# Kernel optimization log

Hardware: AMD Instinct MI355X
Metric: run time of the kernel (lower is better)

Reference implementation:

```python
import jax, jax.numpy as jnp
import numpy as np

B, M, H, NLAYERS = 32768, 32, 64, 4
DIM_IN = (4 + 1) * M  # 160


def prelu(x, a):
    return jnp.where(x >= 0, x, a * x)


def setup_inputs() -> dict:
    key = jax.random.key(0)
    ks = jax.random.split(key, 10)

    x = jax.random.normal(ks[0], (B, M, 4), dtype=jnp.float32)
    pad_mask = jax.random.randint(ks[1], (B, M), 0, 2).astype(bool)

    def lin(k, fan_out, fan_in):
        bound = 1.0 / np.sqrt(fan_in)
        kw, kb = jax.random.split(k)
        W = jax.random.uniform(kw, (fan_out, fan_in), jnp.float32, -bound, bound)
        b = jax.random.uniform(kb, (fan_out,), jnp.float32, -bound, bound)
        return W, b

    W_in, b_in = lin(ks[2], H, DIM_IN)
    a_in = jnp.full((1,), 0.25, jnp.float32)  # PReLU slope

    enc_W, enc_b = [], []
    for i in range(NLAYERS):
        W, b = lin(ks[3 + i], H, H)
        enc_W.append(W)
        enc_b.append(b)
    W_enc = jnp.stack(enc_W)              # [4, 64, 64]
    b_enc = jnp.stack(enc_b)              # [4, 64]
    a_enc = jnp.full((NLAYERS, 1), 0.25, jnp.float32)

    W_out, b_out = lin(ks[8], M, H)       # [32, 64]

    return {"x": x, "pad_mask": pad_mask, "W_in": W_in, "b_in": b_in,
            "a_in": a_in, "W_enc": W_enc, "b_enc": b_enc, "a_enc": a_enc,
            "W_out": W_out, "b_out": b_out}


def reference(x, pad_mask, W_in, b_in, a_in, W_enc, b_enc, a_enc, W_out, b_out):
    # ---- FullyConnectedNetwork: learn per-satellite weights w [B, M] ----
    valid = (~pad_mask).astype(x.dtype)[..., None]          # [B, M, 1]
    feats = jnp.concatenate([x, valid], axis=-1)            # [B, M, 5]
    feats = feats.reshape(feats.shape[0], -1)               # [B, 5*M] (M == max_sats, pad is no-op)

    h = prelu(feats @ W_in.T + b_in, a_in)                  # [B, 64]
    for i in range(NLAYERS):
        h = prelu(h @ W_enc[i].T + b_enc[i], a_enc[i])
    w = h @ W_out.T + b_out                                  # [B, M]

    # ---- Weighted least squares: diag(w) applied as row-scale (same math as diag_embed + bmm) ----
    ones = jnp.ones(x.shape[:2] + (1,), dtype=x.dtype)
    A = jnp.concatenate([-x[:, :, 1:4], ones], axis=-1)      # [B, M, 4]
    r = x[:, :, 0:1]                                         # [B, M, 1]

    WA = w[:, :, None] * A                                   # [B, M, 4]
    Wr = w[:, :, None] * r                                   # [B, M, 1]

    WA_pinv = jnp.linalg.pinv(WA)                            # [B, 4, M]
    out = jnp.matmul(WA_pinv, Wr)[..., 0]                    # [B, 4]
    return out
```

## Files before the change

kernel.cpp:

```cpp
#include <hip/hip_runtime.h>
#include <cstddef>
#include <cstdint>

typedef float f32x4 __attribute__((ext_vector_type(4)));
typedef __bf16 bf16x8 __attribute__((ext_vector_type(8)));

#define MFMA_B16(a, b, c) __builtin_amdgcn_mfma_f32_16x16x32_bf16(a, b, c, 0, 0, 0)

#define OFF_L0   0u
#define OFF_WV   32768u
#define OFF_ENC  40960u
#define OFF_OUT  106496u
#define WS_NEED  114688u

#define XB_OFF   0
#define AH_OFF   32768
#define AL_OFF   40960
#define WG_OFF   49152

__device__ __forceinline__ int xadr(int e, int b) { return (e << 9) | (b ^ ((e & 7) << 4)); }
__device__ __forceinline__ int aadr(int e, int b) { return (e << 7) | (b ^ ((e & 7) << 4)); }

__global__ __launch_bounds__(256)
void prep_frags(const float* __restrict__ W_in, const float* __restrict__ W_enc,
                const float* __restrict__ W_out, unsigned* __restrict__ P) {
  const int idx = blockIdx.x * 256 + threadIdx.x;
  if (idx >= 28672) return;
  const int t = idx & 3;
  const int lane = (idx >> 2) & 63;
  const int g = lane >> 4, c = lane & 15;
  const int j0 = t << 1;
  int pl;
  float w0, w1;
  if (idx < 8192) {
    const int rest = idx >> 8;
    pl = rest & 1;
    const int nt = (rest >> 1) & 3;
    const int kt = rest >> 3;
    const int n = 4 * c + nt;
    const int k = kt * 32 + g * 8 + j0;
    const int m = k >> 2, q = k & 3;
    w0 = W_in[n * 160 + 5 * m + q];
    w1 = W_in[n * 160 + 5 * m + q + 1];
  } else if (idx < 10240) {
    const int rest = (idx - 8192) >> 8;
    pl = rest & 1;
    const int nt = rest >> 1;
    const int n = 4 * c + nt;
    const int m = g * 8 + j0;
    w0 = W_in[n * 160 + 5 * m + 4];
    w1 = W_in[n * 160 + 5 * (m + 1) + 4];
  } else if (idx < 26624) {
    const int rel = idx - 10240;
    const int l = rel >> 12;
    const int rest = (rel & 4095) >> 8;
    pl = rest & 1;
    const int nt = (rest >> 1) & 3;
    const int kt = rest >> 3;
    const int n = 4 * c + nt;
    const int k = kt * 32 + g * 8 + j0;
    w0 = W_enc[(l * 64 + n) * 64 + k];
    w1 = W_enc[(l * 64 + n) * 64 + k + 1];
  } else {
    const int rel = idx - 26624;
    const int rest = rel >> 8;
    pl = rest & 1;
    const int nt = (rest >> 1) & 1;
    const int kt = rest >> 2;
    const int mcol = 16 * nt + c;
    const int k = kt * 32 + g * 8 + j0;
    w0 = W_out[mcol * 64 + k];
    w1 = W_out[mcol * 64 + k + 1];
  }
  unsigned short u0, u1;
  if (pl == 0) {
    u0 = __builtin_bit_cast(unsigned short, (__bf16)w0);
    u1 = __builtin_bit_cast(unsigned short, (__bf16)w1);
  } else {
    const __bf16 h0 = (__bf16)w0, h1 = (__bf16)w1;
    u0 = __builtin_bit_cast(unsigned short, (__bf16)(w0 - (float)h0));
    u1 = __builtin_bit_cast(unsigned short, (__bf16)(w1 - (float)h1));
  }
  P[idx] = (unsigned)u0 | ((unsigned)u1 << 16);
}

__global__ __launch_bounds__(256, 2)
void wls_mfma(const float* __restrict__ x, const int* __restrict__ pad,
              const float* __restrict__ b_in, const float* __restrict__ a_in,
              const float* __restrict__ b_enc, const float* __restrict__ a_enc,
              const float* __restrict__ b_out, const char* __restrict__ wf,
              float* __restrict__ out) {
  __shared__ __align__(16) unsigned char smem[65536];
  const int tid = threadIdx.x;
  const int wave = tid >> 6, lane = tid & 63;
  const int g = lane >> 4, c = lane & 15;
  const int eb = blockIdx.x << 6;
  const int ew = eb + (wave << 4);

  {
    float4 xv[8];
    const char* src = (const char*)x + (size_t)ew * 512 + lane * 16;
    #pragma unroll
    for (int i = 0; i < 8; ++i) xv[i] = *(const float4*)(src + i * 1024);
    #pragma unroll
    for (int i = 0; i < 8; ++i) {
      const int off = i * 1024 + lane * 16;
      const int e = (wave << 4) + (off >> 9);
      *(float4*)(smem + XB_OFF + xadr(e, off & 511)) = xv[i];
    }
  }
  {
    #pragma unroll
    for (int t = 0; t < 2; ++t) {
      const int el = lane >> 2;
      const int mq = (lane & 3) + (t << 2);
      const int4 pv = *(const int4*)(pad + (size_t)(ew + el) * 32 + (mq << 2));
      const unsigned ONE = 0x3F80u;
      const unsigned u0 = (pv.x ? 0u : ONE) | ((pv.y ? 0u : ONE) << 16);
      const unsigned u1 = (pv.z ? 0u : ONE) | ((pv.w ? 0u : ONE) << 16);
      const int e = (wave << 4) + el;
      *(uint2*)(smem + AL_OFF + aadr(e, mq << 3)) = make_uint2(u0, u1);
    }
  }

  auto copy_wgt = [&](unsigned goff, int nbytes) {
    const int share = nbytes >> 2;
    const char* s = wf + goff + wave * share + lane * 16;
    unsigned char* d = smem + WG_OFF + wave * share + lane * 16;
    if (nbytes == 16384) {
      float4 t0 = *(const float4*)(s);
      float4 t1 = *(const float4*)(s + 1024);
      float4 t2 = *(const float4*)(s + 2048);
      float4 t3 = *(const float4*)(s + 3072);
      *(float4*)(d) = t0;           *(float4*)(d + 1024) = t1;
      *(float4*)(d + 2048) = t2;    *(float4*)(d + 3072) = t3;
    } else {
      float4 t0 = *(const float4*)(s);
      float4 t1 = *(const float4*)(s + 1024);
      *(float4*)(d) = t0;           *(float4*)(d + 1024) = t1;
    }
  };
  auto bfrag = [&](int slot) -> bf16x8 {
    return *(const bf16x8*)(smem + WG_OFF + slot * 1024 + lane * 16);
  };
  auto xfrag = [&](int kt, bf16x8& ah, bf16x8& al) {
    const int e = (wave << 4) + c;
    const int b0 = kt * 128 + g * 32;
    const float4 v0 = *(const float4*)(smem + XB_OFF + xadr(e, b0));
    const float4 v1 = *(const float4*)(smem + XB_OFF + xadr(e, b0 + 16));
    const float vv[8] = {v0.x, v0.y, v0.z, v0.w, v1.x, v1.y, v1.z, v1.w};
    #pragma unroll
    for (int j = 0; j < 8; ++j) {
      const __bf16 h = (__bf16)vv[j];
      ah[j] = h;
      al[j] = (__bf16)(vv[j] - (float)h);
    }
  };
  auto act_store = [&](f32x4* a4, float alpha) {
    #pragma unroll
    for (int r = 0; r < 4; ++r) {
      const int e = (wave << 4) + (g << 2) + r;
      unsigned hu[2], lu[2];
      #pragma unroll
      for (int q = 0; q < 2; ++q) {
        unsigned short hb[2], lb[2];
        #pragma unroll
        for (int s2 = 0; s2 < 2; ++s2) {
          float h = a4[2 * q + s2][r];
          h = (h >= 0.0f) ? h : alpha * h;
          const __bf16 hh = (__bf16)h;
          const __bf16 ll = (__bf16)(h - (float)hh);
          hb[s2] = __builtin_bit_cast(unsigned short, hh);
          lb[s2] = __builtin_bit_cast(unsigned short, ll);
        }
        hu[q] = (unsigned)hb[0] | ((unsigned)hb[1] << 16);
        lu[q] = (unsigned)lb[0] | ((unsigned)lb[1] << 16);
      }
      *(uint2*)(smem + AH_OFF + aadr(e, c * 8)) = make_uint2(hu[0], hu[1]);
      *(uint2*)(smem + AL_OFF + aadr(e, c * 8)) = make_uint2(lu[0], lu[1]);
    }
  };

  f32x4 acc[4];
  #pragma unroll
  for (int nt = 0; nt < 4; ++nt) {
    const float bv = b_in[4 * c + nt];
    f32x4 a = {bv, bv, bv, bv};
    acc[nt] = a;
  }
  copy_wgt(OFF_L0, 16384);
  __syncthreads();
  #pragma unroll
  for (int half = 0; half < 2; ++half) {
    if (half) {
      __syncthreads();
      copy_wgt(OFF_L0 + 16384, 16384);
      __syncthreads();
    }
    #pragma unroll
    for (int ktl = 0; ktl < 2; ++ktl) {
      bf16x8 ah, al;
      xfrag(half * 2 + ktl, ah, al);
      #pragma unroll
      for (int nt = 0; nt < 4; ++nt) {
        const bf16x8 bh = bfrag((ktl * 4 + nt) * 2);
        const bf16x8 bl = bfrag((ktl * 4 + nt) * 2 + 1);
        acc[nt] = MFMA_B16(ah, bh, acc[nt]);
        acc[nt] = MFMA_B16(ah, bl, acc[nt]);
        acc[nt] = MFMA_B16(al, bh, acc[nt]);
      }
    }
  }
  __syncthreads();
  copy_wgt(OFF_WV, 8192);
  __syncthreads();
  {
    const int e = (wave << 4) + c;
    const bf16x8 va = *(const bf16x8*)(smem + AL_OFF + aadr(e, g * 16));
    #pragma unroll
    for (int nt = 0; nt < 4; ++nt) {
      const bf16x8 bh = bfrag(nt * 2);
      const bf16x8 bl = bfrag(nt * 2 + 1);
      acc[nt] = MFMA_B16(va, bh, acc[nt]);
      acc[nt] = MFMA_B16(va, bl, acc[nt]);
    }
  }
  act_store(acc, a_in[0]);

  #pragma unroll
  for (int l = 0; l < 4; ++l) {
    __syncthreads();
    copy_wgt(OFF_ENC + l * 16384, 16384);
    __syncthreads();
    bf16x8 ah0, ah1, al0, al1;
    {
      const int e = (wave << 4) + c;
      ah0 = *(const bf16x8*)(smem + AH_OFF + aadr(e, g * 16));
      ah1 = *(const bf16x8*)(smem + AH_OFF + aadr(e, 64 + g * 16));
      al0 = *(const bf16x8*)(smem + AL_OFF + aadr(e, g * 16));
      al1 = *(const bf16x8*)(smem + AL_OFF + aadr(e, 64 + g * 16));
    }
    f32x4 a2[4];
    #pragma unroll
    for (int nt = 0; nt < 4; ++nt) {
      const float bv = b_enc[l * 64 + 4 * c + nt];
      f32x4 a = {bv, bv, bv, bv};
      a2[nt] = a;
    }
    #pragma unroll
    for (int kt = 0; kt < 2; ++kt) {
      const bf16x8 Ah = kt ? ah1 : ah0;
      const bf16x8 Al = kt ? al1 : al0;
      #pragma unroll
      for (int nt = 0; nt < 4; ++nt) {
        const bf16x8 bh = bfrag((kt * 4 + nt) * 2);
        const bf16x8 bl = bfrag((kt * 4 + nt) * 2 + 1);
        a2[nt] = MFMA_B16(Ah, bh, a2[nt]);
        a2[nt] = MFMA_B16(Ah, bl, a2[nt]);
        a2[nt] = MFMA_B16(Al, bh, a2[nt]);
      }
    }
    act_store(a2, a_enc[l]);
  }

  __syncthreads();
  copy_wgt(OFF_OUT, 8192);
  __syncthreads();
  bf16x8 oah[2], oal[2], obh[4], obl[4];
  {
    const int e = (wave << 4) + c;
    #pragma unroll
    for (int kt = 0; kt < 2; ++kt) {
      oah[kt] = *(const bf16x8*)(smem + AH_OFF + aadr(e, kt * 64 + g * 16));
      oal[kt] = *(const bf16x8*)(smem + AL_OFF + aadr(e, kt * 64 + g * 16));
      #pragma unroll
      for (int nt = 0; nt < 2; ++nt) {
        obh[kt * 2 + nt] = bfrag((kt * 2 + nt) * 2);
        obl[kt * 2 + nt] = bfrag((kt * 2 + nt) * 2 + 1);
      }
    }
  }
  __syncthreads();
  f32x4 aw[2];
  #pragma unroll
  for (int nt = 0; nt < 2; ++nt) {
    const float bv = b_out[16 * nt + c];
    f32x4 a = {bv, bv, bv, bv};
    aw[nt] = a;
  }
  #pragma unroll
  for (int kt = 0; kt < 2; ++kt) {
    #pragma unroll
    for (int nt = 0; nt < 2; ++nt) {
      aw[nt] = MFMA_B16(oah[kt], obh[kt * 2 + nt], aw[nt]);
      aw[nt] = MFMA_B16(oah[kt], obl[kt * 2 + nt], aw[nt]);
      aw[nt] = MFMA_B16(oal[kt], obh[kt * 2 + nt], aw[nt]);
    }
  }
  {
    float* ws = (float*)(smem + WG_OFF);
    #pragma unroll
    for (int nt = 0; nt < 2; ++nt)
      #pragma unroll
      for (int r = 0; r < 4; ++r)
        ws[((wave << 4) + (g << 2) + r) * 33 + 16 * nt + c] = aw[nt][r];
  }

  {
    const int el = lane >> 2;
    const int p = lane & 3;
    const int e = (wave << 4) + el;
    const float* ws = (const float*)(smem + WG_OFF);
    float s[14];
    #pragma unroll
    for (int v = 0; v < 14; ++v) s[v] = 0.0f;
    #pragma unroll
    for (int t = 0; t < 8; ++t) {
      const int mm = (p << 3) + t;
      const float w = ws[e * 33 + mm];
      const float4 xv = *(const float4*)(smem + XB_OFF + xadr(e, mm << 4));
      const float r = xv.x;
      const float a1 = -xv.y, a2 = -xv.z, a3 = -xv.w;
      const float ww = w * w;
      const float w1 = ww * a1, w2 = ww * a2, w3 = ww * a3;
      s[0] += w1 * a1;  s[1] += w1 * a2;  s[2] += w1 * a3;  s[3] += w1;
      s[4] += w2 * a2;  s[5] += w2 * a3;  s[6] += w2;
      s[7] += w3 * a3;  s[8] += w3;
      s[9] += ww;
      s[10] += w1 * r;  s[11] += w2 * r;  s[12] += w3 * r;  s[13] += ww * r;
    }
    #pragma unroll
    for (int v = 0; v < 14; ++v) {
      s[v] += __shfl_xor(s[v], 1);
      s[v] += __shfl_xor(s[v], 2);
    }
    float Mt[4][5] = {
      {s[0], s[1], s[2], s[3], s[10]},
      {s[1], s[4], s[5], s[6], s[11]},
      {s[2], s[5], s[7], s[8], s[12]},
      {s[3], s[6], s[8], s[9], s[13]},
    };
    #pragma unroll
    for (int k = 0; k < 3; ++k) {
      const float inv = 1.0f / Mt[k][k];
      #pragma unroll
      for (int r2 = k + 1; r2 < 4; ++r2) {
        const float fk = Mt[r2][k] * inv;
        #pragma unroll
        for (int cc = k + 1; cc < 5; ++cc) Mt[r2][cc] -= fk * Mt[k][cc];
      }
    }
    const float th3 = Mt[3][4] / Mt[3][3];
    const float th2 = (Mt[2][4] - Mt[2][3] * th3) / Mt[2][2];
    const float th1 = (Mt[1][4] - Mt[1][3] * th3 - Mt[1][2] * th2) / Mt[1][1];
    const float th0 = (Mt[0][4] - Mt[0][3] * th3 - Mt[0][2] * th2 - Mt[0][1] * th1) / Mt[0][0];
    if (p == 0) {
      *(float4*)(out + (size_t)(eb + (wave << 4) + el) * 4) = make_float4(th0, th1, th2, th3);
    }
  }
}

extern "C" void kernel_launch(void* const* d_in, const int* in_sizes, int n_in,
                              void* d_out, int out_size, void* d_ws, size_t ws_size,
                              hipStream_t stream) {
  const float* x     = (const float*)d_in[0];
  const int*   pad   = (const int*)d_in[1];
  const float* W_in  = (const float*)d_in[2];
  const float* b_in  = (const float*)d_in[3];
  const float* a_in  = (const float*)d_in[4];
  const float* W_enc = (const float*)d_in[5];
  const float* b_enc = (const float*)d_in[6];
  const float* a_enc = (const float*)d_in[7];
  const float* W_out = (const float*)d_in[8];
  const float* b_out = (const float*)d_in[9];
  float* out = (float*)d_out;

  prep_frags<<<112, 256, 0, stream>>>(W_in, W_enc, W_out, (unsigned*)d_ws);
  wls_mfma<<<512, 256, 0, stream>>>(x, pad, b_in, a_in, b_enc, a_enc, b_out,
                                    (const char*)d_ws, out);
}
```

Measured before the change: 94.77 us.

## Use single-wave blocks reading weight fragments directly from global memory

Shrinks the block from four waves to one wave handling 16 elements and launches four times as many blocks. Weight fragments are no longer staged through LDS with block barriers; each MFMA operand is loaded straight from global memory, relying on L1/L2 caching. This cuts LDS use to about 14 KB and removes all __syncthreads, aiming for higher occupancy and less barrier stalling. The cost is more global and cache traffic for the weight fragments, since every wave fetches them independently.

```diff
diff --git a/kernel.cpp b/kernel.cpp
--- a/kernel.cpp
+++ b/kernel.cpp
@@ -11,12 +11,12 @@
 #define OFF_WV   32768u
 #define OFF_ENC  40960u
 #define OFF_OUT  106496u
-#define WS_NEED  114688u
 
 #define XB_OFF   0
-#define AH_OFF   32768
-#define AL_OFF   40960
-#define WG_OFF   49152
+#define AH_OFF   8192
+#define AL_OFF   10240
+#define WS_OFF   12288
+#define SMEM_SZ  14400
 
 __device__ __forceinline__ int xadr(int e, int b) { return (e << 9) | (b ^ ((e & 7) << 4)); }
 __device__ __forceinline__ int aadr(int e, int b) { return (e << 7) | (b ^ ((e & 7) << 4)); }
@@ -84,18 +84,16 @@
   P[idx] = (unsigned)u0 | ((unsigned)u1 << 16);
 }
 
-__global__ __launch_bounds__(256, 2)
+__global__ __launch_bounds__(64)
 void wls_mfma(const float* __restrict__ x, const int* __restrict__ pad,
               const float* __restrict__ b_in, const float* __restrict__ a_in,
               const float* __restrict__ b_enc, const float* __restrict__ a_enc,
               const float* __restrict__ b_out, const char* __restrict__ wf,
               float* __restrict__ out) {
-  __shared__ __align__(16) unsigned char smem[65536];
-  const int tid = threadIdx.x;
-  const int wave = tid >> 6, lane = tid & 63;
+  __shared__ __align__(16) unsigned char smem[SMEM_SZ];
+  const int lane = threadIdx.x;
   const int g = lane >> 4, c = lane & 15;
-  const int eb = blockIdx.x << 6;
-  const int ew = eb + (wave << 4);
+  const int ew = blockIdx.x << 4;
 
   {
     float4 xv[8];
@@ -105,8 +103,7 @@
     #pragma unroll
     for (int i = 0; i < 8; ++i) {
       const int off = i * 1024 + lane * 16;
-      const int e = (wave << 4) + (off >> 9);
-      *(float4*)(smem + XB_OFF + xadr(e, off & 511)) = xv[i];
+      *(float4*)(smem + XB_OFF + xadr(off >> 9, off & 511)) = xv[i];
     }
   }
   {
@@ -118,36 +115,17 @@
       const unsigned ONE = 0x3F80u;
       const unsigned u0 = (pv.x ? 0u : ONE) | ((pv.y ? 0u : ONE) << 16);
       const unsigned u1 = (pv.z ? 0u : ONE) | ((pv.w ? 0u : ONE) << 16);
-      const int e = (wave << 4) + el;
-      *(uint2*)(smem + AL_OFF + aadr(e, mq << 3)) = make_uint2(u0, u1);
-    }
-  }
-
-  auto copy_wgt = [&](unsigned goff, int nbytes) {
-    const int share = nbytes >> 2;
-    const char* s = wf + goff + wave * share + lane * 16;
-    unsigned char* d = smem + WG_OFF + wave * share + lane * 16;
-    if (nbytes == 16384) {
-      float4 t0 = *(const float4*)(s);
-      float4 t1 = *(const float4*)(s + 1024);
-      float4 t2 = *(const float4*)(s + 2048);
-      float4 t3 = *(const float4*)(s + 3072);
-      *(float4*)(d) = t0;           *(float4*)(d + 1024) = t1;
-      *(float4*)(d + 2048) = t2;    *(float4*)(d + 3072) = t3;
-    } else {
-      float4 t0 = *(const float4*)(s);
-      float4 t1 = *(const float4*)(s + 1024);
-      *(float4*)(d) = t0;           *(float4*)(d + 1024) = t1;
-    }
-  };
-  auto bfrag = [&](int slot) -> bf16x8 {
-    return *(const bf16x8*)(smem + WG_OFF + slot * 1024 + lane * 16);
+      *(uint2*)(smem + AL_OFF + aadr(el, mq << 3)) = make_uint2(u0, u1);
+    }
+  }
+
+  auto bfragG = [&](unsigned goff, int slot) -> bf16x8 {
+    return *(const bf16x8*)(wf + goff + slot * 1024 + lane * 16);
   };
   auto xfrag = [&](int kt, bf16x8& ah, bf16x8& al) {
-    const int e = (wave << 4) + c;
     const int b0 = kt * 128 + g * 32;
-    const float4 v0 = *(const float4*)(smem + XB_OFF + xadr(e, b0));
-    const float4 v1 = *(const float4*)(smem + XB_OFF + xadr(e, b0 + 16));
+    const float4 v0 = *(const float4*)(smem + XB_OFF + xadr(c, b0));
+    const float4 v1 = *(const float4*)(smem + XB_OFF + xadr(c, b0 + 16));
     const float vv[8] = {v0.x, v0.y, v0.z, v0.w, v1.x, v1.y, v1.z, v1.w};
     #pragma unroll
     for (int j = 0; j < 8; ++j) {
@@ -159,7 +137,7 @@
   auto act_store = [&](f32x4* a4, float alpha) {
     #pragma unroll
     for (int r = 0; r < 4; ++r) {
-      const int e = (wave << 4) + (g << 2) + r;
+      const int e = (g << 2) + r;
       unsigned hu[2], lu[2];
       #pragma unroll
       for (int q = 0; q < 2; ++q) {
@@ -188,39 +166,25 @@
     f32x4 a = {bv, bv, bv, bv};
     acc[nt] = a;
   }
-  copy_wgt(OFF_L0, 16384);
-  __syncthreads();
-  #pragma unroll
-  for (int half = 0; half < 2; ++half) {
-    if (half) {
-      __syncthreads();
-      copy_wgt(OFF_L0 + 16384, 16384);
-      __syncthreads();
-    }
-    #pragma unroll
-    for (int ktl = 0; ktl < 2; ++ktl) {
-      bf16x8 ah, al;
-      xfrag(half * 2 + ktl, ah, al);
-      #pragma unroll
-      for (int nt = 0; nt < 4; ++nt) {
-        const bf16x8 bh = bfrag((ktl * 4 + nt) * 2);
-        const bf16x8 bl = bfrag((ktl * 4 + nt) * 2 + 1);
-        acc[nt] = MFMA_B16(ah, bh, acc[nt]);
-        acc[nt] = MFMA_B16(ah, bl, acc[nt]);
-        acc[nt] = MFMA_B16(al, bh, acc[nt]);
-      }
-    }
-  }
-  __syncthreads();
-  copy_wgt(OFF_WV, 8192);
-  __syncthreads();
-  {
-    const int e = (wave << 4) + c;
-    const bf16x8 va = *(const bf16x8*)(smem + AL_OFF + aadr(e, g * 16));
+  #pragma unroll
+  for (int kt = 0; kt < 4; ++kt) {
+    bf16x8 ah, al;
+    xfrag(kt, ah, al);
     #pragma unroll
     for (int nt = 0; nt < 4; ++nt) {
-      const bf16x8 bh = bfrag(nt * 2);
-      const bf16x8 bl = bfrag(nt * 2 + 1);
+      const bf16x8 bh = bfragG(OFF_L0, (kt * 4 + nt) * 2);
+      const bf16x8 bl = bfragG(OFF_L0, (kt * 4 + nt) * 2 + 1);
+      acc[nt] = MFMA_B16(ah, bh, acc[nt]);
+      acc[nt] = MFMA_B16(ah, bl, acc[nt]);
+      acc[nt] = MFMA_B16(al, bh, acc[nt]);
+    }
+  }
+  {
+    const bf16x8 va = *(const bf16x8*)(smem + AL_OFF + aadr(c, g * 16));
+    #pragma unroll
+    for (int nt = 0; nt < 4; ++nt) {
+      const bf16x8 bh = bfragG(OFF_WV, nt * 2);
+      const bf16x8 bl = bfragG(OFF_WV, nt * 2 + 1);
       acc[nt] = MFMA_B16(va, bh, acc[nt]);
       acc[nt] = MFMA_B16(va, bl, acc[nt]);
     }
@@ -229,17 +193,10 @@
 
   #pragma unroll
   for (int l = 0; l < 4; ++l) {
-    __syncthreads();
-    copy_wgt(OFF_ENC + l * 16384, 16384);
-    __syncthreads();
-    bf16x8 ah0, ah1, al0, al1;
-    {
-      const int e = (wave << 4) + c;
-      ah0 = *(const bf16x8*)(smem + AH_OFF + aadr(e, g * 16));
-      ah1 = *(const bf16x8*)(smem + AH_OFF + aadr(e, 64 + g * 16));
-      al0 = *(const bf16x8*)(smem + AL_OFF + aadr(e, g * 16));
-      al1 = *(const bf16x8*)(smem + AL_OFF + aadr(e, 64 + g * 16));
-    }
+    bf16x8 ah0 = *(const bf16x8*)(smem + AH_OFF + aadr(c, g * 16));
+    bf16x8 ah1 = *(const bf16x8*)(smem + AH_OFF + aadr(c, 64 + g * 16));
+    bf16x8 al0 = *(const bf16x8*)(smem + AL_OFF + aadr(c, g * 16));
+    bf16x8 al1 = *(const bf16x8*)(smem + AL_OFF + aadr(c, 64 + g * 16));
     f32x4 a2[4];
     #pragma unroll
     for (int nt = 0; nt < 4; ++nt) {
@@ -253,8 +210,8 @@
       const bf16x8 Al = kt ? al1 : al0;
       #pragma unroll
       for (int nt = 0; nt < 4; ++nt) {
-        const bf16x8 bh = bfrag((kt * 4 + nt) * 2);
-        const bf16x8 bl = bfrag((kt * 4 + nt) * 2 + 1);
+        const bf16x8 bh = bfragG(OFF_ENC + l * 16384, (kt * 4 + nt) * 2);
+        const bf16x8 bl = bfragG(OFF_ENC + l * 16384, (kt * 4 + nt) * 2 + 1);
         a2[nt] = MFMA_B16(Ah, bh, a2[nt]);
         a2[nt] = MFMA_B16(Ah, bl, a2[nt]);
         a2[nt] = MFMA_B16(Al, bh, a2[nt]);
@@ -263,24 +220,6 @@
     act_store(a2, a_enc[l]);
   }
 
-  __syncthreads();
-  copy_wgt(OFF_OUT, 8192);
-  __syncthreads();
-  bf16x8 oah[2], oal[2], obh[4], obl[4];
-  {
-    const int e = (wave << 4) + c;
-    #pragma unroll
-    for (int kt = 0; kt < 2; ++kt) {
-      oah[kt] = *(const bf16x8*)(smem + AH_OFF + aadr(e, kt * 64 + g * 16));
-      oal[kt] = *(const bf16x8*)(smem + AL_OFF + aadr(e, kt * 64 + g * 16));
-      #pragma unroll
-      for (int nt = 0; nt < 2; ++nt) {
-        obh[kt * 2 + nt] = bfrag((kt * 2 + nt) * 2);
-        obl[kt * 2 + nt] = bfrag((kt * 2 + nt) * 2 + 1);
-      }
-    }
-  }
-  __syncthreads();
   f32x4 aw[2];
   #pragma unroll
   for (int nt = 0; nt < 2; ++nt) {
@@ -290,35 +229,38 @@
   }
   #pragma unroll
   for (int kt = 0; kt < 2; ++kt) {
+    const bf16x8 oah = *(const bf16x8*)(smem + AH_OFF + aadr(c, kt * 64 + g * 16));
+    const bf16x8 oal = *(const bf16x8*)(smem + AL_OFF + aadr(c, kt * 64 + g * 16));
     #pragma unroll
     for (int nt = 0; nt < 2; ++nt) {
-      aw[nt] = MFMA_B16(oah[kt], obh[kt * 2 + nt], aw[nt]);
-      aw[nt] = MFMA_B16(oah[kt], obl[kt * 2 + nt], aw[nt]);
-      aw[nt] = MFMA_B16(oal[kt], obh[kt * 2 + nt], aw[nt]);
-    }
-  }
-  {
-    float* ws = (float*)(smem + WG_OFF);
+      const bf16x8 obh = bfragG(OFF_OUT, (kt * 2 + nt) * 2);
+      const bf16x8 obl = bfragG(OFF_OUT, (kt * 2 + nt) * 2 + 1);
+      aw[nt] = MFMA_B16(oah, obh, aw[nt]);
+      aw[nt] = MFMA_B16(oah, obl, aw[nt]);
+      aw[nt] = MFMA_B16(oal, obh, aw[nt]);
+    }
+  }
+  {
+    float* ws = (float*)(smem + WS_OFF);
     #pragma unroll
     for (int nt = 0; nt < 2; ++nt)
       #pragma unroll
       for (int r = 0; r < 4; ++r)
-        ws[((wave << 4) + (g << 2) + r) * 33 + 16 * nt + c] = aw[nt][r];
+        ws[((g << 2) + r) * 33 + 16 * nt + c] = aw[nt][r];
   }
 
   {
     const int el = lane >> 2;
     const int p = lane & 3;
-    const int e = (wave << 4) + el;
-    const float* ws = (const float*)(smem + WG_OFF);
+    const float* ws = (const float*)(smem + WS_OFF);
     float s[14];
     #pragma unroll
     for (int v = 0; v < 14; ++v) s[v] = 0.0f;
     #pragma unroll
     for (int t = 0; t < 8; ++t) {
       const int mm = (p << 3) + t;
-      const float w = ws[e * 33 + mm];
-      const float4 xv = *(const float4*)(smem + XB_OFF + xadr(e, mm << 4));
+      const float w = ws[el * 33 + mm];
+      const float4 xv = *(const float4*)(smem + XB_OFF + xadr(el, mm << 4));
       const float r = xv.x;
       const float a1 = -xv.y, a2 = -xv.z, a3 = -xv.w;
       const float ww = w * w;
@@ -355,7 +297,7 @@
     const float th1 = (Mt[1][4] - Mt[1][3] * th3 - Mt[1][2] * th2) / Mt[1][1];
     const float th0 = (Mt[0][4] - Mt[0][3] * th3 - Mt[0][2] * th2 - Mt[0][1] * th1) / Mt[0][0];
     if (p == 0) {
-      *(float4*)(out + (size_t)(eb + (wave << 4) + el) * 4) = make_float4(th0, th1, th2, th3);
+      *(float4*)(out + (size_t)(ew + el) * 4) = make_float4(th0, th1, th2, th3);
     }
   }
 }
@@ -376,6 +318,6 @@
   float* out = (float*)d_out;
 
   prep_frags<<<112, 256, 0, stream>>>(W_in, W_enc, W_out, (unsigned*)d_ws);
-  wls_mfma<<<512, 256, 0, stream>>>(x, pad, b_in, a_in, b_enc, a_enc, b_out,
+  wls_mfma<<<2048, 64, 0, stream>>>(x, pad, b_in, a_in, b_enc, a_enc, b_out,
                                     (const char*)d_ws, out);
 }
```

Result: slower. 96.71 us (+2.1%).
